# Kernel tuning notes

Measured on AMD Instinct MI355X. Metric: run time of the kernel, lower is better.

Reference implementation:

```python
import jax, jax.numpy as jnp
import numpy as np

B, L, W, K, G = 8, 2048, 1024, 5, 2
OFFSET_SCALE = 2.0
EPS = 1e-5


def setup_inputs() -> dict:
    key = jax.random.key(0)
    ks = jax.random.split(key, 6)
    x = jax.random.normal(ks[0], (B, L, W), jnp.float32)
    # True = padded position
    lengths = jax.random.randint(ks[1], (B,), L // 2, L + 1)
    mask = jnp.arange(L)[None, :] >= lengths[:, None]
    # offset predictor (pointwise): one fractional offset per kernel tap
    w_off = jax.random.normal(ks[2], (W, K), jnp.float32) * 0.02
    b_off = jnp.zeros((K,), jnp.float32)
    # grouped conv weights: [groups, out_per_group, in_per_group, K]
    conv_w = jax.random.normal(ks[3], (G, W // G, W // G, K), jnp.float32) * 0.02
    conv_b = jnp.zeros((W,), jnp.float32)
    gamma = jnp.ones((W,), jnp.float32)
    beta = jnp.zeros((W,), jnp.float32)
    proj_w = jax.random.normal(ks[4], (W,), jnp.float32) * 0.02
    proj_b = jnp.zeros((), jnp.float32)
    return dict(x=x, mask=mask, w_off=w_off, b_off=b_off, conv_w=conv_w,
                conv_b=conv_b, gamma=gamma, beta=beta, proj_w=proj_w, proj_b=proj_b)


def _deform_conv1d(x, w_off, b_off, conv_w, conv_b):
    # x: [B, L, W]; returns [B, L, W]
    Bb, Ll, Ww = x.shape
    Gg, Co, Ci, Kk = conv_w.shape
    # per-position, per-tap fractional offsets in [-offset_scale, offset_scale]
    offsets = jnp.tanh(x @ w_off + b_off) * OFFSET_SCALE            # [B, L, K]
    taps = jnp.arange(Kk, dtype=x.dtype) - (Kk - 1) / 2.0           # centered taps
    pos = jnp.arange(Ll, dtype=x.dtype)[None, :, None] + taps[None, None, :] + offsets  # [B,L,K]
    p0 = jnp.floor(pos)
    frac = pos - p0                                                  # [B, L, K]
    p0i = p0.astype(jnp.int32)
    bidx = jnp.arange(Bb)[:, None, None]

    def gather(idx):
        valid = (idx >= 0) & (idx < Ll)                              # zero padding outside
        samp = x[bidx, jnp.clip(idx, 0, Ll - 1)]                     # [B, L, K, W]
        return samp * valid[..., None].astype(x.dtype)

    # linear interpolation between floor and floor+1 samples
    samp = gather(p0i) * (1.0 - frac)[..., None] + gather(p0i + 1) * frac[..., None]
    samp = samp.reshape(Bb, Ll, Kk, Gg, Ci)                          # split channels into groups
    out = jnp.einsum('blkgc,gock->blgo', samp, conv_w).reshape(Bb, Ll, Gg * Co)
    return out + conv_b


def reference(x, mask, w_off, b_off, conv_w, conv_b, gamma, beta, proj_w, proj_b):
    h = _deform_conv1d(x, w_off, b_off, conv_w, conv_b)              # [B, L, W]
    # LayerNorm over width
    mu = jnp.mean(h, axis=-1, keepdims=True)
    var = jnp.mean((h - mu) ** 2, axis=-1, keepdims=True)
    h = (h - mu) * jax.lax.rsqrt(var + EPS) * gamma + beta
    # dropout is identity in eval mode
    h = jnp.where(mask[..., None], 0.0, h)                           # masked fill
    lengths = jnp.maximum(jnp.sum(~mask, axis=1, keepdims=True).astype(h.dtype), 1.0)
    pooled = jnp.sum(h, axis=1) / lengths                            # [B, W]
    return pooled @ proj_w + proj_b                                  # [B]
```

## Files before the change

### kernel.cpp

```cpp
#include <hip/hip_runtime.h>
#include <hip/hip_bf16.h>

constexpr int Bb = 8, Ll = 2048, Ww = 1024;
constexpr int BL = Bb * Ll;

typedef short bf16x8 __attribute__((ext_vector_type(8)));
typedef float f32x4  __attribute__((ext_vector_type(4)));

__device__ inline unsigned short f2bf(float f) {
    union { float f; unsigned u; } v; v.f = f;
    unsigned u = v.u;
    unsigned r = (u + 0x7fffu + ((u >> 16) & 1u)) >> 16;
    return (unsigned short)r;
}
__device__ inline unsigned lerp_pair(unsigned pa, unsigned pb, float w0, float w1) {
    union { unsigned u; float f; } alo, ahi, blo, bhi;
    alo.u = pa << 16;  ahi.u = pa & 0xffff0000u;
    blo.u = pb << 16;  bhi.u = pb & 0xffff0000u;
    float hlo = w0 * alo.f + w1 * blo.f;
    float hhi = w0 * ahi.f + w1 * bhi.f;
    union { __hip_bfloat162 h2; unsigned u; } r;
    r.h2 = __float22bfloat162_rn(float2{hlo, hhi});
    return r.u;
}

__device__ inline void gl_lds16(const unsigned short* g, unsigned short* l) {
    __builtin_amdgcn_global_load_lds(
        (const __attribute__((address_space(1))) unsigned int*)g,
        (__attribute__((address_space(3))) unsigned int*)l, 16, 0, 0);
}

__global__ void maskA_kernel(const void* __restrict__ mraw, int* __restrict__ flags) {
    const unsigned char* mb = (const unsigned char*)mraw;
    const unsigned* mw = (const unsigned*)mraw;
    int gid = blockIdx.x * 256 + threadIdx.x;
    int nonint = 0, notf = 0, hasf = 0;
    for (int i = gid; i < BL; i += 4096) { if ((i & 3) && mb[i]) nonint = 1; }
    for (int i = gid; i < BL / 4; i += 4096) {
        unsigned w = mw[i];
        if (w == 0x3f800000u) hasf = 1; else if (w) notf = 1;
    }
    if (nonint) atomicOr(&flags[0], 1);
    if (notf)   atomicOr(&flags[1], 1);
    if (hasf)   atomicOr(&flags[2], 1);
}
__global__ void maskB_kernel(const void* __restrict__ mraw, const int* __restrict__ flags,
                             float* __restrict__ maskf) {
    const unsigned char* mb = (const unsigned char*)mraw;
    const unsigned* mw = (const unsigned*)mraw;
    int gid = blockIdx.x * 256 + threadIdx.x;
    int is_f32  = (!flags[1]) && flags[2];
    int is_bool = (!is_f32) && flags[0];
    for (int i = gid; i < BL; i += 4096) {
        int masked = is_bool ? (mb[i] != 0) : (mw[i] != 0u);
        maskf[i] = masked ? 0.0f : 1.0f;
    }
}

__global__ __launch_bounds__(256) void wconv_kernel(const float* __restrict__ conv_w,
                                                    unsigned short* __restrict__ w_t) {
    int t = blockIdx.x * 256 + threadIdx.x;
    int oct = t & 63;
    int o   = (t >> 6) & 511;
    int g   = t >> 15;
    const float* src = conv_w + ((size_t)(g * 512 + o) * 512 + oct * 8) * 5;
    float f[40];
    #pragma unroll
    for (int j = 0; j < 10; j++) *(float4*)&f[j * 4] = *(const float4*)&src[j * 4];
    int r = o & 127, ob = o >> 7, cs = oct >> 2, q = oct & 3;
    int base16 = ((g * 20 + ob) * 16 + cs) * 512 + r * 4 + (q ^ (r & 3));
    #pragma unroll
    for (int k = 0; k < 5; k++) {
        ushort4 lo, hi;
        lo.x = f2bf(f[0 * 5 + k]); lo.y = f2bf(f[1 * 5 + k]);
        lo.z = f2bf(f[2 * 5 + k]); lo.w = f2bf(f[3 * 5 + k]);
        hi.x = f2bf(f[4 * 5 + k]); hi.y = f2bf(f[5 * 5 + k]);
        hi.z = f2bf(f[6 * 5 + k]); hi.w = f2bf(f[7 * 5 + k]);
        int dst16 = base16 + k * 4 * 16 * 512;
        *(ushort4*)&w_t[(size_t)dst16 * 8]     = lo;
        *(ushort4*)&w_t[(size_t)dst16 * 8 + 4] = hi;
    }
}

__global__ __launch_bounds__(256) void offsets_kernel(
    const float* __restrict__ x, const float* __restrict__ w_off, const float* __restrict__ b_off,
    unsigned short* __restrict__ x_bf, float4* __restrict__ pk)
{
    const int wave = threadIdx.x >> 6, lane = threadIdx.x & 63;
    const int bl = blockIdx.x * 4 + wave;
    const int l = bl & (Ll - 1);
    const int c0 = lane * 16;

    const float* xr = x + (size_t)bl * Ww + c0;
    float4 v0 = *(const float4*)(xr + 0);
    float4 v1 = *(const float4*)(xr + 4);
    float4 v2 = *(const float4*)(xr + 8);
    float4 v3 = *(const float4*)(xr + 12);
    float xv[16] = { v0.x,v0.y,v0.z,v0.w, v1.x,v1.y,v1.z,v1.w,
                     v2.x,v2.y,v2.z,v2.w, v3.x,v3.y,v3.z,v3.w };

    uint4 pa, pb;
    unsigned* pu = (unsigned*)&pa;
    #pragma unroll
    for (int j = 0; j < 4; j++) pu[j] = (unsigned)f2bf(xv[j*2]) | ((unsigned)f2bf(xv[j*2+1]) << 16);
    pu = (unsigned*)&pb;
    #pragma unroll
    for (int j = 0; j < 4; j++) pu[j] = (unsigned)f2bf(xv[8+j*2]) | ((unsigned)f2bf(xv[8+j*2+1]) << 16);
    *(uint4*)&x_bf[(size_t)bl * Ww + c0]     = pa;
    *(uint4*)&x_bf[(size_t)bl * Ww + c0 + 8] = pb;

    float acc[5] = {0.f, 0.f, 0.f, 0.f, 0.f};
    const float* wp = w_off + (size_t)c0 * 5;
    #pragma unroll
    for (int j = 0; j < 16; j++) {
        #pragma unroll
        for (int k = 0; k < 5; k++) acc[k] += xv[j] * wp[j * 5 + k];
    }
    #pragma unroll
    for (int k = 0; k < 5; k++)
        #pragma unroll
        for (int off = 32; off; off >>= 1) acc[k] += __shfl_xor(acc[k], off);

    if (lane < 5) {
        float s = (lane == 0) ? acc[0] : (lane == 1) ? acc[1] : (lane == 2) ? acc[2]
                : (lane == 3) ? acc[3] : acc[4];
        s += b_off[lane];
        float offv = tanhf(s) * 2.0f;
        float pos = (float)l + (float)(lane - 2) + offv;
        float p0 = floorf(pos);
        float frac = pos - p0;
        int i0 = (int)p0;
        int i1 = i0 + 1;
        int ok0 = (i0 >= 0) && (i0 < Ll);
        int ok1 = (i1 >= 0) && (i1 < Ll);
        float4 pkv;
        pkv.x = __int_as_float(min(max(i0, 0), Ll - 1));
        pkv.y = __int_as_float(min(max(i1, 0), Ll - 1));
        pkv.z = ok0 ? (1.0f - frac) : 0.0f;
        pkv.w = ok1 ? frac : 0.0f;
        pk[bl * 5 + lane] = pkv;
    }
}

__global__ __launch_bounds__(256, 2) void gemm_kernel(
    const unsigned short* __restrict__ x_bf, const unsigned short* __restrict__ w_t,
    const float4* __restrict__ pk, const float* __restrict__ conv_b,
    unsigned short* __restrict__ h)
{
    __shared__ unsigned short Bs[2][2 * 4096];
    __shared__ unsigned short As[2][4096];
    const int tid = threadIdx.x;
    const int mt = blockIdx.x;
    const int nhalf = blockIdx.y;
    const int g = blockIdx.z;
    const int b = mt >> 4;
    const int lane = tid & 63, wave = tid >> 6;
    const int wr4 = (wave >> 1) * 4;
    const int imgsel = wave & 1;
    const int l15 = lane & 15, l4 = lane >> 4;
    const int sw = (l4 ^ (l15 & 3)) * 8;

    const int arow = ((tid >> 6) << 4) + (tid & 15);
    const int oct8 = ((tid >> 4) & 3) * 8;
    const int bl_a = mt * 128 + arow;
    const int bl_b = bl_a + 64;
    const int gbase = g * 512;

    unsigned off0a, off1a, off0b, off1b;
    float w0a, w1a, w0b, w1b;
    auto load_meta = [&](int k2) {
        float4 pa = pk[bl_a * 5 + k2];
        float4 pb = pk[bl_b * 5 + k2];
        off0a = (unsigned)(((b << 11) + __float_as_int(pa.x)) * Ww + gbase);
        off1a = (unsigned)(((b << 11) + __float_as_int(pa.y)) * Ww + gbase);
        w0a = pa.z; w1a = pa.w;
        off0b = (unsigned)(((b << 11) + __float_as_int(pb.x)) * Ww + gbase);
        off1b = (unsigned)(((b << 11) + __float_as_int(pb.y)) * Ww + gbase);
        w0b = pb.z; w1b = pb.w;
    };
    auto build_A = [&](int cs2, unsigned short* dst) {
        const int ch = cs2 * 32 + oct8;
        uint4 ua = *(const uint4*)(x_bf + off0a + ch);
        uint4 ub = *(const uint4*)(x_bf + off1a + ch);
        uint4 uc = *(const uint4*)(x_bf + off0b + ch);
        uint4 ud = *(const uint4*)(x_bf + off1b + ch);
        uint4 ra, rb;
        ra.x = lerp_pair(ua.x, ub.x, w0a, w1a);
        ra.y = lerp_pair(ua.y, ub.y, w0a, w1a);
        ra.z = lerp_pair(ua.z, ub.z, w0a, w1a);
        ra.w = lerp_pair(ua.w, ub.w, w0a, w1a);
        rb.x = lerp_pair(uc.x, ud.x, w0b, w1b);
        rb.y = lerp_pair(uc.y, ud.y, w0b, w1b);
        rb.z = lerp_pair(uc.z, ud.z, w0b, w1b);
        rb.w = lerp_pair(uc.w, ud.w, w0b, w1b);
        *(uint4*)&dst[tid * 8]         = ra;
        *(uint4*)&dst[(tid + 256) * 8] = rb;
    };

    {
        const int nt0 = nhalf * 2;
        const unsigned short* W0 = w_t + ((size_t)((g * 20 + nt0) * 16 + 0)) * 4096;
        const unsigned short* W1 = w_t + ((size_t)((g * 20 + nt0 + 1) * 16 + 0)) * 4096;
        gl_lds16(W0 + tid * 8,        &Bs[0][tid * 8]);
        gl_lds16(W0 + 2048 + tid * 8, &Bs[0][2048 + tid * 8]);
        gl_lds16(W1 + tid * 8,        &Bs[0][4096 + tid * 8]);
        gl_lds16(W1 + 2048 + tid * 8, &Bs[0][4096 + 2048 + tid * 8]);
    }
    load_meta(0);
    build_A(0, &As[0][0]);
    __syncthreads();

    f32x4 acc[4][8];
    #pragma unroll
    for (int i = 0; i < 4; i++)
        #pragma unroll
        for (int j = 0; j < 8; j++) acc[i][j] = (f32x4){0.f, 0.f, 0.f, 0.f};

    int buf = 0;
    for (int it = 0; it < 80; ++it) {
        const int it2 = it + 1;
        if (it2 < 80) {
            const int k2 = it2 >> 4, cs2 = it2 & 15;
            const int nt0 = k2 * 4 + nhalf * 2;
            const unsigned short* W0 = w_t + ((size_t)((g * 20 + nt0) * 16 + cs2)) * 4096;
            const unsigned short* W1 = w_t + ((size_t)((g * 20 + nt0 + 1) * 16 + cs2)) * 4096;
            unsigned short* bd = &Bs[buf ^ 1][0];
            gl_lds16(W0 + tid * 8,        bd + tid * 8);
            gl_lds16(W0 + 2048 + tid * 8, bd + 2048 + tid * 8);
            gl_lds16(W1 + tid * 8,        bd + 4096 + tid * 8);
            gl_lds16(W1 + 2048 + tid * 8, bd + 4096 + 2048 + tid * 8);
            if (cs2 == 0) load_meta(k2);
            build_A(cs2, &As[buf ^ 1][0]);
        }
        {
            bf16x8 af[4];
            #pragma unroll
            for (int i = 0; i < 4; i++)
                af[i] = *(const bf16x8*)&As[buf][((wr4 + i) * 64 + lane) * 8];
            const unsigned short* bsrc = &Bs[buf][imgsel * 4096];
            #pragma unroll
            for (int j = 0; j < 8; j++) {
                bf16x8 bj = *(const bf16x8*)&bsrc[(j * 16 + l15) * 32 + sw];
                #pragma unroll
                for (int i = 0; i < 4; i++)
                    acc[i][j] = __builtin_amdgcn_mfma_f32_16x16x32_bf16(af[i], bj, acc[i][j], 0, 0, 0);
            }
        }
        __syncthreads();
        buf ^= 1;
    }

    #pragma unroll
    for (int j = 0; j < 8; j++) {
        const int col = g * 512 + nhalf * 256 + imgsel * 128 + j * 16 + l15;
        const float bias = conv_b[col];
        #pragma unroll
        for (int i = 0; i < 4; i++) {
            const int row0 = mt * 128 + (wave >> 1) * 64 + i * 16 + l4 * 4;
            #pragma unroll
            for (int rr = 0; rr < 4; rr++)
                h[(size_t)(row0 + rr) * Ww + col] = f2bf(acc[i][j][rr] + bias);
        }
    }
}

__global__ __launch_bounds__(256) void lnpool_kernel(
    const unsigned short* __restrict__ h, const float* __restrict__ gamma,
    const float* __restrict__ maskf, float* __restrict__ pooled)
{
    const int tid = threadIdx.x;
    const int wave = tid >> 6, lane = tid & 63;
    const int c0 = lane * 16;
    const int bl0 = blockIdx.x * 16 + wave * 4;
    const int b = bl0 >> 11;

    float g16[16];
    #pragma unroll
    for (int j = 0; j < 4; j++) {
        float4 gv = *(const float4*)(gamma + c0 + j * 4);
        g16[j*4+0] = gv.x; g16[j*4+1] = gv.y; g16[j*4+2] = gv.z; g16[j*4+3] = gv.w;
    }
    float pacc[16];
    #pragma unroll
    for (int j = 0; j < 16; j++) pacc[j] = 0.f;

    #pragma unroll
    for (int r = 0; r < 4; r++) {
        const int bl = bl0 + r;
        const float m = maskf[bl];
        const uint4 ha = *(const uint4*)(h + (size_t)bl * Ww + c0);
        const uint4 hb = *(const uint4*)(h + (size_t)bl * Ww + c0 + 8);
        float hf[16];
        const unsigned* pw = (const unsigned*)&ha;
        #pragma unroll
        for (int j = 0; j < 4; j++) {
            union { unsigned u; float f; } lo, hi;
            lo.u = pw[j] << 16; hi.u = pw[j] & 0xffff0000u;
            hf[j*2] = lo.f; hf[j*2+1] = hi.f;
        }
        pw = (const unsigned*)&hb;
        #pragma unroll
        for (int j = 0; j < 4; j++) {
            union { unsigned u; float f; } lo, hi;
            lo.u = pw[j] << 16; hi.u = pw[j] & 0xffff0000u;
            hf[8+j*2] = lo.f; hf[8+j*2+1] = hi.f;
        }
        float s1 = 0.f, s2 = 0.f;
        #pragma unroll
        for (int j = 0; j < 16; j++) { s1 += hf[j]; s2 += hf[j] * hf[j]; }
        #pragma unroll
        for (int off = 32; off; off >>= 1) {
            s1 += __shfl_xor(s1, off);
            s2 += __shfl_xor(s2, off);
        }
        const float mu = s1 * (1.0f / 1024.0f);
        const float var = s2 * (1.0f / 1024.0f) - mu * mu;
        const float rstd = rsqrtf(var + 1e-5f) * m;
        #pragma unroll
        for (int j = 0; j < 16; j++) pacc[j] += (hf[j] - mu) * rstd * g16[j];
    }
    __shared__ float spool[4][1024];
    #pragma unroll
    for (int j = 0; j < 4; j++)
        *(float4*)&spool[wave][c0 + j * 4] = *(float4*)&pacc[j * 4];
    __syncthreads();
    const int ch = tid * 4;
    float4 a = *(float4*)&spool[0][ch];
    float4 bq = *(float4*)&spool[1][ch];
    float4 cq = *(float4*)&spool[2][ch];
    float4 dq = *(float4*)&spool[3][ch];
    atomicAdd(&pooled[b * Ww + ch + 0], a.x + bq.x + cq.x + dq.x);
    atomicAdd(&pooled[b * Ww + ch + 1], a.y + bq.y + cq.y + dq.y);
    atomicAdd(&pooled[b * Ww + ch + 2], a.z + bq.z + cq.z + dq.z);
    atomicAdd(&pooled[b * Ww + ch + 3], a.w + bq.w + cq.w + dq.w);
}

__global__ void final_kernel(const float* __restrict__ pooled, const float* __restrict__ maskf,
                             const float* __restrict__ beta, const float* __restrict__ proj_w,
                             const float* __restrict__ proj_b, float* __restrict__ out)
{
    int b = blockIdx.x;
    int tid = threadIdx.x;
    float len = 0.f, dotP = 0.f, dotB = 0.f;
    for (int l = tid; l < Ll; l += 256) len += maskf[b * Ll + l];
    for (int c = tid; c < Ww; c += 256) {
        dotP += pooled[b * Ww + c] * proj_w[c];
        dotB += beta[c] * proj_w[c];
    }
    for (int off = 32; off; off >>= 1) {
        len += __shfl_down(len, off);
        dotP += __shfl_down(dotP, off);
        dotB += __shfl_down(dotB, off);
    }
    __shared__ float rl[4], rp[4], rb[4];
    int wave = tid >> 6, lane = tid & 63;
    if (lane == 0) { rl[wave] = len; rp[wave] = dotP; rb[wave] = dotB; }
    __syncthreads();
    if (tid == 0) {
        float Lt = rl[0] + rl[1] + rl[2] + rl[3];
        float Pt = rp[0] + rp[1] + rp[2] + rp[3];
        float Bt = rb[0] + rb[1] + rb[2] + rb[3];
        out[b] = Pt / fmaxf(Lt, 1.0f) + Bt + proj_b[0];
    }
}


extern "C" void kernel_launch(void* const* d_in, const int* in_sizes, int n_in,
                              void* d_out, int out_size, void* d_ws, size_t ws_size,
                              hipStream_t stream)
{
    const float* x      = (const float*)d_in[0];
    const void*  mask   = d_in[1];
    const float* w_off  = (const float*)d_in[2];
    const float* b_off  = (const float*)d_in[3];
    const float* conv_w = (const float*)d_in[4];
    const float* conv_b = (const float*)d_in[5];
    const float* gamma  = (const float*)d_in[6];
    const float* beta   = (const float*)d_in[7];
    const float* proj_w = (const float*)d_in[8];
    const float* proj_b = (const float*)d_in[9];
    float* out = (float*)d_out;

    char* ws = (char*)d_ws;
    float* maskf         = (float*)(ws + 0);
    float* pooled        = (float*)(ws + 65536);
    int*   flags         = (int*)(ws + 98304);
    float4* pk           = (float4*)(ws + 98320);
    unsigned short* w_t  = (unsigned short*)(ws + 1409040);
    unsigned short* x_bf = (unsigned short*)(ws + 6651920);
    unsigned short* h    = (unsigned short*)(ws + 40206352);

    hipMemsetAsync(pooled, 0, Bb * Ww * sizeof(float), stream);
    hipMemsetAsync(flags, 0, 16, stream);
    maskA_kernel<<<16, 256, 0, stream>>>(mask, flags);
    maskB_kernel<<<16, 256, 0, stream>>>(mask, flags, maskf);
    wconv_kernel<<<256, 256, 0, stream>>>(conv_w, w_t);
    offsets_kernel<<<BL / 4, 256, 0, stream>>>(x, w_off, b_off, x_bf, pk);
    gemm_kernel<<<dim3(128, 2, 2), 256, 0, stream>>>(x_bf, w_t, pk, conv_b, h);
    lnpool_kernel<<<1024, 256, 0, stream>>>(h, gamma, maskf, pooled);
    final_kernel<<<8, 256, 0, stream>>>(pooled, maskf, beta, proj_w, proj_b, out);
}
```

Measured before the change: 321.0 us.

## Restructure GEMM pipeline to overlap gather with MFMA and drop pooling atomics

The GEMM main loop becomes a nested tap/chunk loop. Next-stage gather loads and weight prefetches are issued before the MFMA block, and the lerp plus LDS store run after it, so global load latency overlaps compute. Per-tap offset metadata is prefetched one tap ahead. Separately, the LN-pool kernel writes per-block partial sums into a reused workspace region (aliasing x_bf, which is dead by then) instead of using atomics, so the memset is removed and final_kernel does the reduction. This adds register pressure and relies on x_bf no longer being needed after the GEMM.

```diff
diff --git a/kernel.cpp b/kernel.cpp
--- a/kernel.cpp
+++ b/kernel.cpp
@@ -165,25 +165,35 @@
     const int bl_a = mt * 128 + arow;
     const int bl_b = bl_a + 64;
     const int gbase = g * 512;
+    const int rowbase = (b << 11);
 
     unsigned off0a, off1a, off0b, off1b;
     float w0a, w1a, w0b, w1b;
-    auto load_meta = [&](int k2) {
-        float4 pa = pk[bl_a * 5 + k2];
-        float4 pb = pk[bl_b * 5 + k2];
-        off0a = (unsigned)(((b << 11) + __float_as_int(pa.x)) * Ww + gbase);
-        off1a = (unsigned)(((b << 11) + __float_as_int(pa.y)) * Ww + gbase);
+    unsigned noff0a = 0, noff1a = 0, noff0b = 0, noff1b = 0;
+    float nw0a = 0.f, nw1a = 0.f, nw0b = 0.f, nw1b = 0.f;
+
+    {
+        float4 pa = pk[bl_a * 5 + 0];
+        float4 pb = pk[bl_b * 5 + 0];
+        off0a = (unsigned)((rowbase + __float_as_int(pa.x)) * Ww + gbase);
+        off1a = (unsigned)((rowbase + __float_as_int(pa.y)) * Ww + gbase);
         w0a = pa.z; w1a = pa.w;
-        off0b = (unsigned)(((b << 11) + __float_as_int(pb.x)) * Ww + gbase);
-        off1b = (unsigned)(((b << 11) + __float_as_int(pb.y)) * Ww + gbase);
+        off0b = (unsigned)((rowbase + __float_as_int(pb.x)) * Ww + gbase);
+        off1b = (unsigned)((rowbase + __float_as_int(pb.y)) * Ww + gbase);
         w0b = pb.z; w1b = pb.w;
-    };
-    auto build_A = [&](int cs2, unsigned short* dst) {
-        const int ch = cs2 * 32 + oct8;
-        uint4 ua = *(const uint4*)(x_bf + off0a + ch);
-        uint4 ub = *(const uint4*)(x_bf + off1a + ch);
-        uint4 uc = *(const uint4*)(x_bf + off0b + ch);
-        uint4 ud = *(const uint4*)(x_bf + off1b + ch);
+    }
+    {
+        const int nt0 = nhalf * 2;
+        const unsigned short* W0 = w_t + ((size_t)((g * 20 + nt0) * 16 + 0)) * 4096;
+        const unsigned short* W1 = W0 + 65536;
+        gl_lds16(W0 + tid * 8,        &Bs[0][tid * 8]);
+        gl_lds16(W0 + 2048 + tid * 8, &Bs[0][2048 + tid * 8]);
+        gl_lds16(W1 + tid * 8,        &Bs[0][4096 + tid * 8]);
+        gl_lds16(W1 + 2048 + tid * 8, &Bs[0][4096 + 2048 + tid * 8]);
+        uint4 ua = *(const uint4*)(x_bf + off0a + oct8);
+        uint4 ub = *(const uint4*)(x_bf + off1a + oct8);
+        uint4 uc = *(const uint4*)(x_bf + off0b + oct8);
+        uint4 ud = *(const uint4*)(x_bf + off1b + oct8);
         uint4 ra, rb;
         ra.x = lerp_pair(ua.x, ub.x, w0a, w1a);
         ra.y = lerp_pair(ua.y, ub.y, w0a, w1a);
@@ -193,21 +203,9 @@
         rb.y = lerp_pair(uc.y, ud.y, w0b, w1b);
         rb.z = lerp_pair(uc.z, ud.z, w0b, w1b);
         rb.w = lerp_pair(uc.w, ud.w, w0b, w1b);
-        *(uint4*)&dst[tid * 8]         = ra;
-        *(uint4*)&dst[(tid + 256) * 8] = rb;
-    };
-
-    {
-        const int nt0 = nhalf * 2;
-        const unsigned short* W0 = w_t + ((size_t)((g * 20 + nt0) * 16 + 0)) * 4096;
-        const unsigned short* W1 = w_t + ((size_t)((g * 20 + nt0 + 1) * 16 + 0)) * 4096;
-        gl_lds16(W0 + tid * 8,        &Bs[0][tid * 8]);
-        gl_lds16(W0 + 2048 + tid * 8, &Bs[0][2048 + tid * 8]);
-        gl_lds16(W1 + tid * 8,        &Bs[0][4096 + tid * 8]);
-        gl_lds16(W1 + 2048 + tid * 8, &Bs[0][4096 + 2048 + tid * 8]);
-    }
-    load_meta(0);
-    build_A(0, &As[0][0]);
+        *(uint4*)&As[0][tid * 8]         = ra;
+        *(uint4*)&As[0][(tid + 256) * 8] = rb;
+    }
     __syncthreads();
 
     f32x4 acc[4][8];
@@ -216,38 +214,80 @@
         #pragma unroll
         for (int j = 0; j < 8; j++) acc[i][j] = (f32x4){0.f, 0.f, 0.f, 0.f};
 
-    int buf = 0;
-    for (int it = 0; it < 80; ++it) {
-        const int it2 = it + 1;
-        if (it2 < 80) {
-            const int k2 = it2 >> 4, cs2 = it2 & 15;
-            const int nt0 = k2 * 4 + nhalf * 2;
-            const unsigned short* W0 = w_t + ((size_t)((g * 20 + nt0) * 16 + cs2)) * 4096;
-            const unsigned short* W1 = w_t + ((size_t)((g * 20 + nt0 + 1) * 16 + cs2)) * 4096;
-            unsigned short* bd = &Bs[buf ^ 1][0];
-            gl_lds16(W0 + tid * 8,        bd + tid * 8);
-            gl_lds16(W0 + 2048 + tid * 8, bd + 2048 + tid * 8);
-            gl_lds16(W1 + tid * 8,        bd + 4096 + tid * 8);
-            gl_lds16(W1 + 2048 + tid * 8, bd + 4096 + 2048 + tid * 8);
-            if (cs2 == 0) load_meta(k2);
-            build_A(cs2, &As[buf ^ 1][0]);
-        }
-        {
-            bf16x8 af[4];
-            #pragma unroll
-            for (int i = 0; i < 4; i++)
-                af[i] = *(const bf16x8*)&As[buf][((wr4 + i) * 64 + lane) * 8];
-            const unsigned short* bsrc = &Bs[buf][imgsel * 4096];
-            #pragma unroll
-            for (int j = 0; j < 8; j++) {
-                bf16x8 bj = *(const bf16x8*)&bsrc[(j * 16 + l15) * 32 + sw];
+    for (int k = 0; k < 5; ++k) {
+        if (k < 4) {
+            float4 pa = pk[bl_a * 5 + k + 1];
+            float4 pb = pk[bl_b * 5 + k + 1];
+            noff0a = (unsigned)((rowbase + __float_as_int(pa.x)) * Ww + gbase);
+            noff1a = (unsigned)((rowbase + __float_as_int(pa.y)) * Ww + gbase);
+            nw0a = pa.z; nw1a = pa.w;
+            noff0b = (unsigned)((rowbase + __float_as_int(pb.x)) * Ww + gbase);
+            noff1b = (unsigned)((rowbase + __float_as_int(pb.y)) * Ww + gbase);
+            nw0b = pb.z; nw1b = pb.w;
+        }
+        #pragma unroll
+        for (int cs = 0; cs < 16; ++cs) {
+            const int p = cs & 1;
+            const bool boundary = (cs == 15);
+            const bool last = boundary && (k == 4);
+            uint4 ua, ub, uc, ud;
+            if (!last) {
+                const int cs2 = (cs + 1) & 15;
+                const int ch = cs2 * 32 + oct8;
+                const unsigned o0a = boundary ? noff0a : off0a;
+                const unsigned o1a = boundary ? noff1a : off1a;
+                const unsigned o0b = boundary ? noff0b : off0b;
+                const unsigned o1b = boundary ? noff1b : off1b;
+                ua = *(const uint4*)(x_bf + o0a + ch);
+                ub = *(const uint4*)(x_bf + o1a + ch);
+                uc = *(const uint4*)(x_bf + o0b + ch);
+                ud = *(const uint4*)(x_bf + o1b + ch);
+                const int nt0 = (boundary ? k + 1 : k) * 4 + nhalf * 2;
+                const unsigned short* W0 = w_t + ((size_t)((g * 20 + nt0) * 16 + cs2)) * 4096;
+                const unsigned short* W1 = W0 + 65536;
+                unsigned short* bd = &Bs[p ^ 1][0];
+                gl_lds16(W0 + tid * 8,        bd + tid * 8);
+                gl_lds16(W0 + 2048 + tid * 8, bd + 2048 + tid * 8);
+                gl_lds16(W1 + tid * 8,        bd + 4096 + tid * 8);
+                gl_lds16(W1 + 2048 + tid * 8, bd + 4096 + 2048 + tid * 8);
+            }
+            {
+                bf16x8 af[4];
                 #pragma unroll
                 for (int i = 0; i < 4; i++)
-                    acc[i][j] = __builtin_amdgcn_mfma_f32_16x16x32_bf16(af[i], bj, acc[i][j], 0, 0, 0);
+                    af[i] = *(const bf16x8*)&As[p][((wr4 + i) * 64 + lane) * 8];
+                const unsigned short* bsrc = &Bs[p][imgsel * 4096];
+                #pragma unroll
+                for (int j = 0; j < 8; j++) {
+                    bf16x8 bj = *(const bf16x8*)&bsrc[(j * 16 + l15) * 32 + sw];
+                    #pragma unroll
+                    for (int i = 0; i < 4; i++)
+                        acc[i][j] = __builtin_amdgcn_mfma_f32_16x16x32_bf16(af[i], bj, acc[i][j], 0, 0, 0);
+                }
             }
-        }
-        __syncthreads();
-        buf ^= 1;
+            if (!last) {
+                const float v0a = boundary ? nw0a : w0a;
+                const float v1a = boundary ? nw1a : w1a;
+                const float v0b = boundary ? nw0b : w0b;
+                const float v1b = boundary ? nw1b : w1b;
+                uint4 ra, rb;
+                ra.x = lerp_pair(ua.x, ub.x, v0a, v1a);
+                ra.y = lerp_pair(ua.y, ub.y, v0a, v1a);
+                ra.z = lerp_pair(ua.z, ub.z, v0a, v1a);
+                ra.w = lerp_pair(ua.w, ub.w, v0a, v1a);
+                rb.x = lerp_pair(uc.x, ud.x, v0b, v1b);
+                rb.y = lerp_pair(uc.y, ud.y, v0b, v1b);
+                rb.z = lerp_pair(uc.z, ud.z, v0b, v1b);
+                rb.w = lerp_pair(uc.w, ud.w, v0b, v1b);
+                *(uint4*)&As[p ^ 1][tid * 8]         = ra;
+                *(uint4*)&As[p ^ 1][(tid + 256) * 8] = rb;
+            }
+            __syncthreads();
+            if (boundary && k < 4) {
+                off0a = noff0a; off1a = noff1a; w0a = nw0a; w1a = nw1a;
+                off0b = noff0b; off1b = noff1b; w0b = nw0b; w1b = nw1b;
+            }
+        }
     }
 
     #pragma unroll
@@ -266,13 +306,12 @@
 
 __global__ __launch_bounds__(256) void lnpool_kernel(
     const unsigned short* __restrict__ h, const float* __restrict__ gamma,
-    const float* __restrict__ maskf, float* __restrict__ pooled)
+    const float* __restrict__ maskf, float* __restrict__ partial)
 {
     const int tid = threadIdx.x;
     const int wave = tid >> 6, lane = tid & 63;
     const int c0 = lane * 16;
     const int bl0 = blockIdx.x * 16 + wave * 4;
-    const int b = bl0 >> 11;
 
     float g16[16];
     #pragma unroll
@@ -329,26 +368,32 @@
     float4 bq = *(float4*)&spool[1][ch];
     float4 cq = *(float4*)&spool[2][ch];
     float4 dq = *(float4*)&spool[3][ch];
-    atomicAdd(&pooled[b * Ww + ch + 0], a.x + bq.x + cq.x + dq.x);
-    atomicAdd(&pooled[b * Ww + ch + 1], a.y + bq.y + cq.y + dq.y);
-    atomicAdd(&pooled[b * Ww + ch + 2], a.z + bq.z + cq.z + dq.z);
-    atomicAdd(&pooled[b * Ww + ch + 3], a.w + bq.w + cq.w + dq.w);
-}
-
-__global__ void final_kernel(const float* __restrict__ pooled, const float* __restrict__ maskf,
+    float4 s; s.x = a.x + bq.x + cq.x + dq.x; s.y = a.y + bq.y + cq.y + dq.y;
+    s.z = a.z + bq.z + cq.z + dq.z; s.w = a.w + bq.w + cq.w + dq.w;
+    *(float4*)&partial[(size_t)blockIdx.x * 1024 + ch] = s;
+}
+
+__global__ void final_kernel(const float* __restrict__ partial, const float* __restrict__ maskf,
                              const float* __restrict__ beta, const float* __restrict__ proj_w,
                              const float* __restrict__ proj_b, float* __restrict__ out)
 {
     int b = blockIdx.x;
     int tid = threadIdx.x;
-    float len = 0.f, dotP = 0.f, dotB = 0.f;
+    float len = 0.f;
     for (int l = tid; l < Ll; l += 256) len += maskf[b * Ll + l];
-    for (int c = tid; c < Ww; c += 256) {
-        dotP += pooled[b * Ww + c] * proj_w[c];
-        dotB += beta[c] * proj_w[c];
-    }
+    const int ch = tid * 4;
+    float4 ps = {0.f, 0.f, 0.f, 0.f};
+    #pragma unroll 8
+    for (int j = 0; j < 128; ++j) {
+        float4 v = *(const float4*)&partial[(size_t)((b << 7) + j) * 1024 + ch];
+        ps.x += v.x; ps.y += v.y; ps.z += v.z; ps.w += v.w;
+    }
+    float4 pw = *(const float4*)&proj_w[ch];
+    float4 bt = *(const float4*)&beta[ch];
+    float dotP = ps.x * pw.x + ps.y * pw.y + ps.z * pw.z + ps.w * pw.w;
+    float dotB = bt.x * pw.x + bt.y * pw.y + bt.z * pw.z + bt.w * pw.w;
     for (int off = 32; off; off >>= 1) {
-        len += __shfl_down(len, off);
+        len  += __shfl_down(len, off);
         dotP += __shfl_down(dotP, off);
         dotB += __shfl_down(dotB, off);
     }
@@ -383,20 +428,19 @@
 
     char* ws = (char*)d_ws;
     float* maskf         = (float*)(ws + 0);
-    float* pooled        = (float*)(ws + 65536);
     int*   flags         = (int*)(ws + 98304);
     float4* pk           = (float4*)(ws + 98320);
     unsigned short* w_t  = (unsigned short*)(ws + 1409040);
     unsigned short* x_bf = (unsigned short*)(ws + 6651920);
+    float* partial       = (float*)(ws + 6651920);
     unsigned short* h    = (unsigned short*)(ws + 40206352);
 
-    hipMemsetAsync(pooled, 0, Bb * Ww * sizeof(float), stream);
     hipMemsetAsync(flags, 0, 16, stream);
     maskA_kernel<<<16, 256, 0, stream>>>(mask, flags);
     maskB_kernel<<<16, 256, 0, stream>>>(mask, flags, maskf);
     wconv_kernel<<<256, 256, 0, stream>>>(conv_w, w_t);
     offsets_kernel<<<BL / 4, 256, 0, stream>>>(x, w_off, b_off, x_bf, pk);
     gemm_kernel<<<dim3(128, 2, 2), 256, 0, stream>>>(x_bf, w_t, pk, conv_b, h);
-    lnpool_kernel<<<1024, 256, 0, stream>>>(h, gamma, maskf, pooled);
-    final_kernel<<<8, 256, 0, stream>>>(pooled, maskf, beta, proj_w, proj_b, out);
-}
+    lnpool_kernel<<<1024, 256, 0, stream>>>(h, gamma, maskf, partial);
+    final_kernel<<<8, 256, 0, stream>>>(partial, maskf, beta, proj_w, proj_b, out);
+}
```

Result: no change. 325.6 us (+1.4%).

## Fuse prep kernels into one launch and replace pooled atomics with partial sums

Applied to the files above, without the earlier changes.

Merges the mask-detection, mask-conversion, weight-conversion and offsets kernels into a single prep kernel that picks its role from the block index. The two memsets disappear. The lnpool stage now writes per-block partial sums into the workspace (reusing the x_bf region, which is dead after the GEMM) instead of issuing global atomics. final_kernel reduces those 128 partials per batch itself. This removes several launches and atomic contention, at the cost of 16 mask blocks each redundantly scanning the whole mask to detect its type.

```diff
diff --git a/kernel.cpp b/kernel.cpp
--- a/kernel.cpp
+++ b/kernel.cpp
@@ -30,115 +30,115 @@
         (__attribute__((address_space(3))) unsigned int*)l, 16, 0, 0);
 }
 
-__global__ void maskA_kernel(const void* __restrict__ mraw, int* __restrict__ flags) {
-    const unsigned char* mb = (const unsigned char*)mraw;
-    const unsigned* mw = (const unsigned*)mraw;
-    int gid = blockIdx.x * 256 + threadIdx.x;
-    int nonint = 0, notf = 0, hasf = 0;
-    for (int i = gid; i < BL; i += 4096) { if ((i & 3) && mb[i]) nonint = 1; }
-    for (int i = gid; i < BL / 4; i += 4096) {
-        unsigned w = mw[i];
-        if (w == 0x3f800000u) hasf = 1; else if (w) notf = 1;
-    }
-    if (nonint) atomicOr(&flags[0], 1);
-    if (notf)   atomicOr(&flags[1], 1);
-    if (hasf)   atomicOr(&flags[2], 1);
-}
-__global__ void maskB_kernel(const void* __restrict__ mraw, const int* __restrict__ flags,
-                             float* __restrict__ maskf) {
-    const unsigned char* mb = (const unsigned char*)mraw;
-    const unsigned* mw = (const unsigned*)mraw;
-    int gid = blockIdx.x * 256 + threadIdx.x;
-    int is_f32  = (!flags[1]) && flags[2];
-    int is_bool = (!is_f32) && flags[0];
-    for (int i = gid; i < BL; i += 4096) {
-        int masked = is_bool ? (mb[i] != 0) : (mw[i] != 0u);
-        maskf[i] = masked ? 0.0f : 1.0f;
-    }
-}
-
-__global__ __launch_bounds__(256) void wconv_kernel(const float* __restrict__ conv_w,
-                                                    unsigned short* __restrict__ w_t) {
-    int t = blockIdx.x * 256 + threadIdx.x;
-    int oct = t & 63;
-    int o   = (t >> 6) & 511;
-    int g   = t >> 15;
-    const float* src = conv_w + ((size_t)(g * 512 + o) * 512 + oct * 8) * 5;
-    float f[40];
-    #pragma unroll
-    for (int j = 0; j < 10; j++) *(float4*)&f[j * 4] = *(const float4*)&src[j * 4];
-    int r = o & 127, ob = o >> 7, cs = oct >> 2, q = oct & 3;
-    int base16 = ((g * 20 + ob) * 16 + cs) * 512 + r * 4 + (q ^ (r & 3));
-    #pragma unroll
-    for (int k = 0; k < 5; k++) {
-        ushort4 lo, hi;
-        lo.x = f2bf(f[0 * 5 + k]); lo.y = f2bf(f[1 * 5 + k]);
-        lo.z = f2bf(f[2 * 5 + k]); lo.w = f2bf(f[3 * 5 + k]);
-        hi.x = f2bf(f[4 * 5 + k]); hi.y = f2bf(f[5 * 5 + k]);
-        hi.z = f2bf(f[6 * 5 + k]); hi.w = f2bf(f[7 * 5 + k]);
-        int dst16 = base16 + k * 4 * 16 * 512;
-        *(ushort4*)&w_t[(size_t)dst16 * 8]     = lo;
-        *(ushort4*)&w_t[(size_t)dst16 * 8 + 4] = hi;
-    }
-}
-
-__global__ __launch_bounds__(256) void offsets_kernel(
+__global__ __launch_bounds__(256) void prep_kernel(
     const float* __restrict__ x, const float* __restrict__ w_off, const float* __restrict__ b_off,
-    unsigned short* __restrict__ x_bf, float4* __restrict__ pk)
+    const float* __restrict__ conv_w, const void* __restrict__ mraw,
+    unsigned short* __restrict__ x_bf, float4* __restrict__ pk,
+    unsigned short* __restrict__ w_t, float* __restrict__ maskf)
 {
-    const int wave = threadIdx.x >> 6, lane = threadIdx.x & 63;
-    const int bl = blockIdx.x * 4 + wave;
-    const int l = bl & (Ll - 1);
-    const int c0 = lane * 16;
-
-    const float* xr = x + (size_t)bl * Ww + c0;
-    float4 v0 = *(const float4*)(xr + 0);
-    float4 v1 = *(const float4*)(xr + 4);
-    float4 v2 = *(const float4*)(xr + 8);
-    float4 v3 = *(const float4*)(xr + 12);
-    float xv[16] = { v0.x,v0.y,v0.z,v0.w, v1.x,v1.y,v1.z,v1.w,
-                     v2.x,v2.y,v2.z,v2.w, v3.x,v3.y,v3.z,v3.w };
-
-    uint4 pa, pb;
-    unsigned* pu = (unsigned*)&pa;
-    #pragma unroll
-    for (int j = 0; j < 4; j++) pu[j] = (unsigned)f2bf(xv[j*2]) | ((unsigned)f2bf(xv[j*2+1]) << 16);
-    pu = (unsigned*)&pb;
-    #pragma unroll
-    for (int j = 0; j < 4; j++) pu[j] = (unsigned)f2bf(xv[8+j*2]) | ((unsigned)f2bf(xv[8+j*2+1]) << 16);
-    *(uint4*)&x_bf[(size_t)bl * Ww + c0]     = pa;
-    *(uint4*)&x_bf[(size_t)bl * Ww + c0 + 8] = pb;
-
-    float acc[5] = {0.f, 0.f, 0.f, 0.f, 0.f};
-    const float* wp = w_off + (size_t)c0 * 5;
-    #pragma unroll
-    for (int j = 0; j < 16; j++) {
-        #pragma unroll
-        for (int k = 0; k < 5; k++) acc[k] += xv[j] * wp[j * 5 + k];
-    }
-    #pragma unroll
-    for (int k = 0; k < 5; k++)
-        #pragma unroll
-        for (int off = 32; off; off >>= 1) acc[k] += __shfl_xor(acc[k], off);
-
-    if (lane < 5) {
-        float s = (lane == 0) ? acc[0] : (lane == 1) ? acc[1] : (lane == 2) ? acc[2]
-                : (lane == 3) ? acc[3] : acc[4];
-        s += b_off[lane];
-        float offv = tanhf(s) * 2.0f;
-        float pos = (float)l + (float)(lane - 2) + offv;
-        float p0 = floorf(pos);
-        float frac = pos - p0;
-        int i0 = (int)p0;
-        int i1 = i0 + 1;
-        int ok0 = (i0 >= 0) && (i0 < Ll);
-        int ok1 = (i1 >= 0) && (i1 < Ll);
-        float4 pkv;
-        pkv.x = __int_as_float(min(max(i0, 0), Ll - 1));
-        pkv.y = __int_as_float(min(max(i1, 0), Ll - 1));
-        pkv.z = ok0 ? (1.0f - frac) : 0.0f;
-        pkv.w = ok1 ? frac : 0.0f;
-        pk[bl * 5 + lane] = pkv;
+    const int blk = blockIdx.x;
+    const int tid = threadIdx.x;
+
+    if (blk < 4096) {
+        const int wave = tid >> 6, lane = tid & 63;
+        const int bl = blk * 4 + wave;
+        const int l = bl & (Ll - 1);
+        const int c0 = lane * 16;
+
+        const float* xr = x + (size_t)bl * Ww + c0;
+        float4 v0 = *(const float4*)(xr + 0);
+        float4 v1 = *(const float4*)(xr + 4);
+        float4 v2 = *(const float4*)(xr + 8);
+        float4 v3 = *(const float4*)(xr + 12);
+        float xv[16] = { v0.x,v0.y,v0.z,v0.w, v1.x,v1.y,v1.z,v1.w,
+                         v2.x,v2.y,v2.z,v2.w, v3.x,v3.y,v3.z,v3.w };
+
+        uint4 pa, pb;
+        unsigned* pu = (unsigned*)&pa;
+        #pragma unroll
+        for (int j = 0; j < 4; j++) pu[j] = (unsigned)f2bf(xv[j*2]) | ((unsigned)f2bf(xv[j*2+1]) << 16);
+        pu = (unsigned*)&pb;
+        #pragma unroll
+        for (int j = 0; j < 4; j++) pu[j] = (unsigned)f2bf(xv[8+j*2]) | ((unsigned)f2bf(xv[8+j*2+1]) << 16);
+        *(uint4*)&x_bf[(size_t)bl * Ww + c0]     = pa;
+        *(uint4*)&x_bf[(size_t)bl * Ww + c0 + 8] = pb;
+
+        float acc[5] = {0.f, 0.f, 0.f, 0.f, 0.f};
+        const float* wp = w_off + (size_t)c0 * 5;
+        #pragma unroll
+        for (int j = 0; j < 16; j++) {
+            #pragma unroll
+            for (int k = 0; k < 5; k++) acc[k] += xv[j] * wp[j * 5 + k];
+        }
+        #pragma unroll
+        for (int k = 0; k < 5; k++)
+            #pragma unroll
+            for (int off = 32; off; off >>= 1) acc[k] += __shfl_xor(acc[k], off);
+
+        if (lane < 5) {
+            float s = (lane == 0) ? acc[0] : (lane == 1) ? acc[1] : (lane == 2) ? acc[2]
+                    : (lane == 3) ? acc[3] : acc[4];
+            s += b_off[lane];
+            float offv = tanhf(s) * 2.0f;
+            float pos = (float)l + (float)(lane - 2) + offv;
+            float p0 = floorf(pos);
+            float frac = pos - p0;
+            int i0 = (int)p0;
+            int i1 = i0 + 1;
+            int ok0 = (i0 >= 0) && (i0 < Ll);
+            int ok1 = (i1 >= 0) && (i1 < Ll);
+            float4 pkv;
+            pkv.x = __int_as_float(min(max(i0, 0), Ll - 1));
+            pkv.y = __int_as_float(min(max(i1, 0), Ll - 1));
+            pkv.z = ok0 ? (1.0f - frac) : 0.0f;
+            pkv.w = ok1 ? frac : 0.0f;
+            pk[bl * 5 + lane] = pkv;
+        }
+    } else if (blk < 4352) {
+        int t = (blk - 4096) * 256 + tid;
+        int oct = t & 63;
+        int o   = (t >> 6) & 511;
+        int g   = t >> 15;
+        const float* src = conv_w + ((size_t)(g * 512 + o) * 512 + oct * 8) * 5;
+        float f[40];
+        #pragma unroll
+        for (int j = 0; j < 10; j++) *(float4*)&f[j * 4] = *(const float4*)&src[j * 4];
+        int r = o & 127, ob = o >> 7, cs = oct >> 2, q = oct & 3;
+        int base16 = ((g * 20 + ob) * 16 + cs) * 512 + r * 4 + (q ^ (r & 3));
+        #pragma unroll
+        for (int k = 0; k < 5; k++) {
+            ushort4 lo, hi;
+            lo.x = f2bf(f[0 * 5 + k]); lo.y = f2bf(f[1 * 5 + k]);
+            lo.z = f2bf(f[2 * 5 + k]); lo.w = f2bf(f[3 * 5 + k]);
+            hi.x = f2bf(f[4 * 5 + k]); hi.y = f2bf(f[5 * 5 + k]);
+            hi.z = f2bf(f[6 * 5 + k]); hi.w = f2bf(f[7 * 5 + k]);
+            int dst16 = base16 + k * 4 * 16 * 512;
+            *(ushort4*)&w_t[(size_t)dst16 * 8]     = lo;
+            *(ushort4*)&w_t[(size_t)dst16 * 8 + 4] = hi;
+        }
+    } else {
+        const unsigned char* mb = (const unsigned char*)mraw;
+        const unsigned* mw = (const unsigned*)mraw;
+        int nonint = 0, notf = 0, hasf = 0;
+        for (int i = tid; i < BL; i += 256) { if ((i & 3) && mb[i]) nonint = 1; }
+        for (int i = tid; i < BL / 4; i += 256) {
+            unsigned w = mw[i];
+            if (w == 0x3f800000u) hasf = 1; else if (w) notf = 1;
+        }
+        __shared__ int sf[3];
+        if (tid == 0) { sf[0] = 0; sf[1] = 0; sf[2] = 0; }
+        __syncthreads();
+        if (nonint) atomicOr(&sf[0], 1);
+        if (notf)   atomicOr(&sf[1], 1);
+        if (hasf)   atomicOr(&sf[2], 1);
+        __syncthreads();
+        const int is_f32  = (!sf[1]) && sf[2];
+        const int is_bool = (!is_f32) && sf[0];
+        const int gid = (blk - 4352) * 256 + tid;
+        for (int i = gid; i < BL; i += 4096) {
+            int masked = is_bool ? (mb[i] != 0) : (mw[i] != 0u);
+            maskf[i] = masked ? 0.0f : 1.0f;
+        }
     }
 }
 
@@ -266,13 +266,12 @@
 
 __global__ __launch_bounds__(256) void lnpool_kernel(
     const unsigned short* __restrict__ h, const float* __restrict__ gamma,
-    const float* __restrict__ maskf, float* __restrict__ pooled)
+    const float* __restrict__ maskf, float* __restrict__ partial)
 {
     const int tid = threadIdx.x;
     const int wave = tid >> 6, lane = tid & 63;
     const int c0 = lane * 16;
     const int bl0 = blockIdx.x * 16 + wave * 4;
-    const int b = bl0 >> 11;
 
     float g16[16];
     #pragma unroll
@@ -329,26 +328,32 @@
     float4 bq = *(float4*)&spool[1][ch];
     float4 cq = *(float4*)&spool[2][ch];
     float4 dq = *(float4*)&spool[3][ch];
-    atomicAdd(&pooled[b * Ww + ch + 0], a.x + bq.x + cq.x + dq.x);
-    atomicAdd(&pooled[b * Ww + ch + 1], a.y + bq.y + cq.y + dq.y);
-    atomicAdd(&pooled[b * Ww + ch + 2], a.z + bq.z + cq.z + dq.z);
-    atomicAdd(&pooled[b * Ww + ch + 3], a.w + bq.w + cq.w + dq.w);
-}
-
-__global__ void final_kernel(const float* __restrict__ pooled, const float* __restrict__ maskf,
+    float4 s; s.x = a.x + bq.x + cq.x + dq.x; s.y = a.y + bq.y + cq.y + dq.y;
+    s.z = a.z + bq.z + cq.z + dq.z; s.w = a.w + bq.w + cq.w + dq.w;
+    *(float4*)&partial[(size_t)blockIdx.x * 1024 + ch] = s;
+}
+
+__global__ void final_kernel(const float* __restrict__ partial, const float* __restrict__ maskf,
                              const float* __restrict__ beta, const float* __restrict__ proj_w,
                              const float* __restrict__ proj_b, float* __restrict__ out)
 {
     int b = blockIdx.x;
     int tid = threadIdx.x;
-    float len = 0.f, dotP = 0.f, dotB = 0.f;
+    float len = 0.f;
     for (int l = tid; l < Ll; l += 256) len += maskf[b * Ll + l];
-    for (int c = tid; c < Ww; c += 256) {
-        dotP += pooled[b * Ww + c] * proj_w[c];
-        dotB += beta[c] * proj_w[c];
-    }
+    const int ch = tid * 4;
+    float4 ps = {0.f, 0.f, 0.f, 0.f};
+    #pragma unroll 8
+    for (int j = 0; j < 128; ++j) {
+        float4 v = *(const float4*)&partial[(size_t)((b << 7) + j) * 1024 + ch];
+        ps.x += v.x; ps.y += v.y; ps.z += v.z; ps.w += v.w;
+    }
+    float4 pw = *(const float4*)&proj_w[ch];
+    float4 bt = *(const float4*)&beta[ch];
+    float dotP = ps.x * pw.x + ps.y * pw.y + ps.z * pw.z + ps.w * pw.w;
+    float dotB = bt.x * pw.x + bt.y * pw.y + bt.z * pw.z + bt.w * pw.w;
     for (int off = 32; off; off >>= 1) {
-        len += __shfl_down(len, off);
+        len  += __shfl_down(len, off);
         dotP += __shfl_down(dotP, off);
         dotB += __shfl_down(dotB, off);
     }
@@ -383,20 +388,15 @@
 
     char* ws = (char*)d_ws;
     float* maskf         = (float*)(ws + 0);
-    float* pooled        = (float*)(ws + 65536);
-    int*   flags         = (int*)(ws + 98304);
     float4* pk           = (float4*)(ws + 98320);
     unsigned short* w_t  = (unsigned short*)(ws + 1409040);
     unsigned short* x_bf = (unsigned short*)(ws + 6651920);
+    float* partial       = (float*)(ws + 6651920);
     unsigned short* h    = (unsigned short*)(ws + 40206352);
 
-    hipMemsetAsync(pooled, 0, Bb * Ww * sizeof(float), stream);
-    hipMemsetAsync(flags, 0, 16, stream);
-    maskA_kernel<<<16, 256, 0, stream>>>(mask, flags);
-    maskB_kernel<<<16, 256, 0, stream>>>(mask, flags, maskf);
-    wconv_kernel<<<256, 256, 0, stream>>>(conv_w, w_t);
-    offsets_kernel<<<BL / 4, 256, 0, stream>>>(x, w_off, b_off, x_bf, pk);
+    prep_kernel<<<4368, 256, 0, stream>>>(x, w_off, b_off, conv_w, mask,
+                                          x_bf, pk, w_t, maskf);
     gemm_kernel<<<dim3(128, 2, 2), 256, 0, stream>>>(x_bf, w_t, pk, conv_b, h);
-    lnpool_kernel<<<1024, 256, 0, stream>>>(h, gamma, maskf, pooled);
-    final_kernel<<<8, 256, 0, stream>>>(pooled, maskf, beta, proj_w, proj_b, out);
-}
+    lnpool_kernel<<<1024, 256, 0, stream>>>(h, gamma, maskf, partial);
+    final_kernel<<<8, 256, 0, stream>>>(partial, maskf, beta, proj_w, proj_b, out);
+}
```

Measured after the change: 311.5 us. 1.03x faster.
